# Kernel optimization log

Measured on AMD Instinct MI355X. Metric: run time of the kernel, lower is better.

## Reference

```python
import jax, jax.numpy as jnp
import numpy as np

H, B, S, D, T = 4, 16, 2048, 128, 5  # n_head, batch, seq_len, d_model, num event types
BAND_K = 64  # latest-k band width, as in get_latest_k_mask


def setup_inputs() -> dict:
    key = jax.random.key(0)
    ks = jax.random.split(key, 5)
    output = jax.random.normal(ks[0], (B, S, D), dtype=jnp.float32)
    # banded 'latest-k' mask: mask[i, i:i+k] = 1  (start=max(i,i-k+1)=i, end=min(S,i+k))
    i = jnp.arange(S)
    band = ((i[None, :] >= i[:, None]) & (i[None, :] < i[:, None] + BAND_K)).astype(jnp.float32)
    local_cor = band[None]  # [1, S, S]
    cor_matrix = jax.random.normal(ks[1], (T, D), dtype=jnp.float32)
    event_type = jax.random.randint(ks[2], (B, S), 1, T + 1)  # 1-based event ids in [1, T]
    # per-head linear3 params (xavier-ish); self.linear is unused in forward
    W3 = jax.random.normal(ks[3], (H, D, D), dtype=jnp.float32) / np.sqrt(D)
    b3 = jnp.zeros((H, D), dtype=jnp.float32)
    return dict(output=output, local_cor=local_cor, cor_matrix=cor_matrix,
                event_type=event_type, W3=W3, b3=b3)


def reference(output, local_cor, cor_matrix, event_type, W3, b3):
    # (corr^T @ cor_matrix[et-1]).mean(2) == einsum('bsd,bs->bd', corr, cor_matrix[et-1].mean(-1))
    g = cor_matrix.mean(-1)[event_type - 1]  # [B, S]
    x = output
    sum_seq = jnp.zeros_like(output)          # sum over heads of [B,S,D]
    sum_head = jnp.zeros((output.shape[0], output.shape[2]), output.dtype)  # [B,D]
    for h in range(H):
        z = jax.nn.elu(jnp.einsum('bsd,ed->bse', x, W3[h]) + b3[h])  # linear3 + ELU
        corr = jnp.matmul(local_cor, z)       # [1,S,S] @ [B,S,D] -> [B,S,D]
        head_out = jnp.einsum('bsd,bs->bd', corr, g)  # [B,D]
        sum_seq = sum_seq + corr
        sum_head = sum_head + head_out
        x = corr                               # next head consumes correlation_output
    return (sum_seq, sum_head)
```

## Files before the change

### kernel.cpp

```cpp
#include <hip/hip_runtime.h>
#include <math.h>

#define NHEAD 4
#define BATCH 16
#define SEQ   2048
#define DMODEL 128
#define NTYPES 5
#define BAND  64
#define MROWS (BATCH * SEQ)

typedef __attribute__((ext_vector_type(8))) short bf16x8;
typedef __attribute__((ext_vector_type(4))) float f32x4;
typedef __attribute__((ext_vector_type(4))) unsigned int u32x4;

static __device__ __forceinline__ unsigned short f2bf(float f) {
  unsigned int u = __float_as_uint(f);
  unsigned int r = (u + 0x7fffu + ((u >> 16) & 1u)) >> 16;
  return (unsigned short)r;
}
static __device__ __forceinline__ float bflo(unsigned int v) {
  return __uint_as_float(v << 16);
}
static __device__ __forceinline__ float bfhi(unsigned int v) {
  return __uint_as_float(v & 0xffff0000u);
}
static __device__ __forceinline__ unsigned int pkbf(float lo, float hi) {
  return ((unsigned int)f2bf(hi) << 16) | (unsigned int)f2bf(lo);
}
static __device__ __forceinline__ int xcd_swz(int blk, int nwg) {
  return (blk & 7) * (nwg >> 3) + (blk >> 3);
}

__global__ __launch_bounds__(512, 4) void gemm0_kernel(
    const float* __restrict__ X0,
    const float* __restrict__ W3h,
    const float* __restrict__ bvec,
    unsigned short* __restrict__ Zb,
    float* __restrict__ SH) {
  __shared__ __align__(16) char lds[64 * 272 + 128 * 272];
  char* Xl = lds;
  char* Wl = lds + 64 * 272;
  const int tid = threadIdx.x;
  const int swz = xcd_swz(blockIdx.x, gridDim.x);
  const int row0 = swz * 64;

  if (blockIdx.x < 16 && tid < DMODEL) SH[blockIdx.x * DMODEL + tid] = 0.f;

  #pragma unroll
  for (int it = 0; it < 2; ++it) {
    const int u = it * 512 + tid;
    const int r = u >> 4, g4 = u & 15;
    const float* xs = X0 + (long)(row0 + r) * DMODEL + g4 * 8;
    float4 f0 = *reinterpret_cast<const float4*>(xs);
    float4 f1 = *reinterpret_cast<const float4*>(xs + 4);
    unsigned short o[8];
    o[0] = f2bf(f0.x); o[1] = f2bf(f0.y); o[2] = f2bf(f0.z); o[3] = f2bf(f0.w);
    o[4] = f2bf(f1.x); o[5] = f2bf(f1.y); o[6] = f2bf(f1.z); o[7] = f2bf(f1.w);
    *reinterpret_cast<u32x4*>(Xl + r * 272 + g4 * 16) = *reinterpret_cast<u32x4*>(o);
  }
  #pragma unroll
  for (int it = 0; it < 4; ++it) {
    const int u = it * 512 + tid;
    const int e = u >> 4, g4 = u & 15;
    const float* wsrc = W3h + e * DMODEL + g4 * 8;
    float4 f0 = *reinterpret_cast<const float4*>(wsrc);
    float4 f1 = *reinterpret_cast<const float4*>(wsrc + 4);
    unsigned short o[8];
    o[0] = f2bf(f0.x); o[1] = f2bf(f0.y); o[2] = f2bf(f0.z); o[3] = f2bf(f0.w);
    o[4] = f2bf(f1.x); o[5] = f2bf(f1.y); o[6] = f2bf(f1.z); o[7] = f2bf(f1.w);
    *reinterpret_cast<u32x4*>(Wl + e * 272 + g4 * 16) = *reinterpret_cast<u32x4*>(o);
  }
  __syncthreads();

  const int wv = tid >> 6, l = tid & 63;
  const int mv = wv >> 1, nh = wv & 1;
  const int lr = l & 15, lk = l >> 4;
  f32x4 acc[4];
  #pragma unroll
  for (int n = 0; n < 4; ++n) acc[n] = (f32x4){0.f, 0.f, 0.f, 0.f};
  #pragma unroll
  for (int t = 0; t < 4; ++t) {
    const bf16x8 a = *reinterpret_cast<const bf16x8*>(
        Xl + (mv * 16 + lr) * 272 + (t * 4 + lk) * 16);
    #pragma unroll
    for (int n = 0; n < 4; ++n) {
      const bf16x8 bfrag = *reinterpret_cast<const bf16x8*>(
          Wl + (nh * 64 + n * 16 + lr) * 272 + (t * 4 + lk) * 16);
      acc[n] = __builtin_amdgcn_mfma_f32_16x16x32_bf16(a, bfrag, acc[n], 0, 0, 0);
    }
  }
  #pragma unroll
  for (int n = 0; n < 4; ++n) {
    const int col = nh * 64 + n * 16 + lr;
    const float bias = bvec[col];
    #pragma unroll
    for (int r = 0; r < 4; ++r) {
      const int row = row0 + mv * 16 + lk * 4 + r;
      float v = acc[n][r] + bias;
      const float e = expm1f(fminf(v, 0.f));
      v = v > 0.f ? v : e;
      Zb[(long)row * DMODEL + col] = f2bf(v);
    }
  }
}

template <int ACC>
__global__ __launch_bounds__(512, 4) void fused_band_gemm(
    const unsigned short* __restrict__ Zin,
    const unsigned short* __restrict__ CSin,
    unsigned short* __restrict__ Cout,
    const float* __restrict__ W3h,
    const float* __restrict__ bvec,
    unsigned short* __restrict__ Zout,
    float* __restrict__ SH,
    const int* __restrict__ et,
    const float* __restrict__ corm) {
  __shared__ __align__(16) char lds[56320];
  __shared__ float g_lds[64];
  __shared__ float rowmean[NTYPES];
  char* Xl = lds;
  char* Wl = lds + 17408;
  float2* s8 = reinterpret_cast<float2*>(lds + 17408);
  float* hred = reinterpret_cast<float*>(lds + 52224);

  const int tid = threadIdx.x;
  const int swz = xcd_swz(blockIdx.x, gridDim.x);
  const int r0 = swz * 64;
  const int b = r0 >> 11, s0 = r0 & 2047;
  const int p = tid & 63, q = tid >> 6;

  const unsigned int* zsrc =
      reinterpret_cast<const unsigned int*>(Zin) + (long)b * SEQ * 64 + p;
  unsigned int zlo[8], zhi[8];
  #pragma unroll
  for (int i = 0; i < 8; ++i) {
    const int sl = s0 + q * 8 + i;
    zlo[i] = zsrc[(long)sl * 64];
    const int sh_ = sl + BAND;
    zhi[i] = (sh_ < SEQ) ? zsrc[(long)sh_ * 64] : 0u;
  }
  unsigned int csr[8];
  if (ACC) {
    #pragma unroll
    for (int i = 0; i < 8; ++i)
      csr[i] = *reinterpret_cast<const unsigned int*>(
          CSin + ((long)r0 + q * 8 + i) * DMODEL + 2 * p);
  }
  u32x4 wfr[4];
  #pragma unroll
  for (int it = 0; it < 4; ++it) {
    const int u = it * 512 + tid;
    const int e = u >> 4, g4 = u & 15;
    const float* wsrc = W3h + e * DMODEL + g4 * 8;
    float4 f0 = *reinterpret_cast<const float4*>(wsrc);
    float4 f1 = *reinterpret_cast<const float4*>(wsrc + 4);
    unsigned short o[8];
    o[0] = f2bf(f0.x); o[1] = f2bf(f0.y); o[2] = f2bf(f0.z); o[3] = f2bf(f0.w);
    o[4] = f2bf(f1.x); o[5] = f2bf(f1.y); o[6] = f2bf(f1.z); o[7] = f2bf(f1.w);
    wfr[it] = *reinterpret_cast<u32x4*>(o);
  }
  int etv = 1;
  if (tid < 64) etv = et[(long)b * SEQ + s0 + tid];
  if (tid < 64) {
    #pragma unroll
    for (int t = 0; t < NTYPES; ++t) {
      float v = corm[t * DMODEL + tid] + corm[t * DMODEL + 64 + tid];
      #pragma unroll
      for (int o = 32; o > 0; o >>= 1) v += __shfl_xor(v, o, 64);
      if (tid == 0) rowmean[t] = v * (1.0f / DMODEL);
    }
  }

  {
    float a0 = 0.f, a1 = 0.f, b0 = 0.f, b1 = 0.f;
    #pragma unroll
    for (int i = 0; i < 8; ++i) {
      a0 += bflo(zlo[i]); a1 += bfhi(zlo[i]);
      b0 += bflo(zhi[i]); b1 += bfhi(zhi[i]);
    }
    s8[q * 64 + p] = make_float2(a0, a1);
    s8[(q + 8) * 64 + p] = make_float2(b0, b1);
  }
  __syncthreads();

  float w0 = 0.f, w1 = 0.f;
  #pragma unroll
  for (int j = 0; j < 8; ++j) {
    const float2 v = s8[(q + j) * 64 + p];
    w0 += v.x; w1 += v.y;
  }
  if (tid < 64) g_lds[tid] = rowmean[etv - 1];
  __syncthreads();

  #pragma unroll
  for (int it = 0; it < 4; ++it) {
    const int u = it * 512 + tid;
    const int e = u >> 4, g4 = u & 15;
    *reinterpret_cast<u32x4*>(Wl + e * 272 + g4 * 16) = wfr[it];
  }
  float hs0 = 0.f, hs1 = 0.f;
  #pragma unroll
  for (int i = 0; i < 8; ++i) {
    const int s = q * 8 + i;
    const float c0v = w0, c1v = w1;
    const float g = g_lds[s];
    hs0 += c0v * g; hs1 += c1v * g;
    unsigned int pk;
    if (ACC)
      pk = pkbf(c0v + bflo(csr[i]), c1v + bfhi(csr[i]));
    else
      pk = pkbf(c0v, c1v);
    *reinterpret_cast<unsigned int*>(Cout + ((long)r0 + s) * DMODEL + 2 * p) = pk;
    *reinterpret_cast<unsigned int*>(Xl + s * 272 + p * 4) =
        ACC ? pkbf(c0v, c1v) : pk;
    w0 += bflo(zhi[i]) - bflo(zlo[i]);
    w1 += bfhi(zhi[i]) - bfhi(zlo[i]);
  }
  *reinterpret_cast<float2*>(hred + (p * 8 + q) * 2) = make_float2(hs0, hs1);
  __syncthreads();

  if (q == 0) {
    float t0 = 0.f, t1 = 0.f;
    #pragma unroll
    for (int k = 0; k < 8; ++k) {
      const float2 v = *reinterpret_cast<const float2*>(hred + (p * 8 + k) * 2);
      t0 += v.x; t1 += v.y;
    }
    atomicAdd(SH + b * DMODEL + 2 * p, t0);
    atomicAdd(SH + b * DMODEL + 2 * p + 1, t1);
  }
  const int wv = tid >> 6, l = tid & 63;
  const int mv = wv >> 1, nh = wv & 1;
  const int lr = l & 15, lk = l >> 4;
  f32x4 acc[4];
  #pragma unroll
  for (int n = 0; n < 4; ++n) acc[n] = (f32x4){0.f, 0.f, 0.f, 0.f};
  #pragma unroll
  for (int t = 0; t < 4; ++t) {
    const bf16x8 a = *reinterpret_cast<const bf16x8*>(
        Xl + (mv * 16 + lr) * 272 + (t * 4 + lk) * 16);
    #pragma unroll
    for (int n = 0; n < 4; ++n) {
      const bf16x8 bfrag = *reinterpret_cast<const bf16x8*>(
          Wl + (nh * 64 + n * 16 + lr) * 272 + (t * 4 + lk) * 16);
      acc[n] = __builtin_amdgcn_mfma_f32_16x16x32_bf16(a, bfrag, acc[n], 0, 0, 0);
    }
  }
  #pragma unroll
  for (int n = 0; n < 4; ++n) {
    const int col = nh * 64 + n * 16 + lr;
    const float bias = bvec[col];
    #pragma unroll
    for (int r = 0; r < 4; ++r) {
      const int row = r0 + mv * 16 + lk * 4 + r;
      float v = acc[n][r] + bias;
      const float e = expm1f(fminf(v, 0.f));
      v = v > 0.f ? v : e;
      Zout[(long)row * DMODEL + col] = f2bf(v);
    }
  }
}

__global__ __launch_bounds__(512, 4) void band3_kernel(
    const unsigned short* __restrict__ Zin,
    const unsigned short* __restrict__ CSin,
    float* __restrict__ SS,
    float* __restrict__ SH,
    const int* __restrict__ et,
    const float* __restrict__ corm) {
  __shared__ float2 s8[16 * 64];
  __shared__ float hred[64 * 8 * 2];
  __shared__ float g_lds[64];
  __shared__ float rowmean[NTYPES];

  const int tid = threadIdx.x;
  const int swz = xcd_swz(blockIdx.x, gridDim.x);
  const int r0 = swz * 64;
  const int b = r0 >> 11, s0 = r0 & 2047;
  const int p = tid & 63, q = tid >> 6;

  const unsigned int* zsrc =
      reinterpret_cast<const unsigned int*>(Zin) + (long)b * SEQ * 64 + p;
  unsigned int zlo[8], zhi[8], csr[8];
  #pragma unroll
  for (int i = 0; i < 8; ++i) {
    const int sl = s0 + q * 8 + i;
    zlo[i] = zsrc[(long)sl * 64];
    const int sh_ = sl + BAND;
    zhi[i] = (sh_ < SEQ) ? zsrc[(long)sh_ * 64] : 0u;
    csr[i] = *reinterpret_cast<const unsigned int*>(
        CSin + ((long)r0 + q * 8 + i) * DMODEL + 2 * p);
  }
  int etv = 1;
  if (tid < 64) etv = et[(long)b * SEQ + s0 + tid];
  if (tid < 64) {
    #pragma unroll
    for (int t = 0; t < NTYPES; ++t) {
      float v = corm[t * DMODEL + tid] + corm[t * DMODEL + 64 + tid];
      #pragma unroll
      for (int o = 32; o > 0; o >>= 1) v += __shfl_xor(v, o, 64);
      if (tid == 0) rowmean[t] = v * (1.0f / DMODEL);
    }
  }
  {
    float a0 = 0.f, a1 = 0.f, b0 = 0.f, b1 = 0.f;
    #pragma unroll
    for (int i = 0; i < 8; ++i) {
      a0 += bflo(zlo[i]); a1 += bfhi(zlo[i]);
      b0 += bflo(zhi[i]); b1 += bfhi(zhi[i]);
    }
    s8[q * 64 + p] = make_float2(a0, a1);
    s8[(q + 8) * 64 + p] = make_float2(b0, b1);
  }
  __syncthreads();

  float w0 = 0.f, w1 = 0.f;
  #pragma unroll
  for (int j = 0; j < 8; ++j) {
    const float2 v = s8[(q + j) * 64 + p];
    w0 += v.x; w1 += v.y;
  }
  if (tid < 64) g_lds[tid] = rowmean[etv - 1];
  __syncthreads();

  float hs0 = 0.f, hs1 = 0.f;
  #pragma unroll
  for (int i = 0; i < 8; ++i) {
    const int s = q * 8 + i;
    const float c0v = w0, c1v = w1;
    const float g = g_lds[s];
    hs0 += c0v * g; hs1 += c1v * g;
    float2 o;
    o.x = c0v + bflo(csr[i]);
    o.y = c1v + bfhi(csr[i]);
    *reinterpret_cast<float2*>(SS + ((long)r0 + s) * DMODEL + 2 * p) = o;
    w0 += bflo(zhi[i]) - bflo(zlo[i]);
    w1 += bfhi(zhi[i]) - bfhi(zlo[i]);
  }
  *reinterpret_cast<float2*>(hred + (p * 8 + q) * 2) = make_float2(hs0, hs1);
  __syncthreads();
  if (q == 0) {
    float t0 = 0.f, t1 = 0.f;
    #pragma unroll
    for (int k = 0; k < 8; ++k) {
      const float2 v = *reinterpret_cast<const float2*>(hred + (p * 8 + k) * 2);
      t0 += v.x; t1 += v.y;
    }
    atomicAdd(SH + b * DMODEL + 2 * p, t0);
    atomicAdd(SH + b * DMODEL + 2 * p + 1, t1);
  }
}

extern "C" void kernel_launch(void* const* d_in, const int* in_sizes, int n_in,
                              void* d_out, int out_size, void* d_ws, size_t ws_size,
                              hipStream_t stream) {
  const float* x0   = (const float*)d_in[0];
  const float* corm = (const float*)d_in[2];
  const int*   et   = (const int*)d_in[3];
  const float* W3   = (const float*)d_in[4];
  const float* b3   = (const float*)d_in[5];

  float* out_ss = (float*)d_out;
  float* out_sh = out_ss + (size_t)MROWS * DMODEL;

  char* ws = (char*)d_ws;
  const size_t MB = 1024 * 1024;
  unsigned short* A = (unsigned short*)(ws + 0 * MB);
  unsigned short* B = (unsigned short*)(ws + 8 * MB);
  unsigned short* C = (unsigned short*)(ws + 16 * MB);
  unsigned short* D = (unsigned short*)(ws + 24 * MB);
  unsigned short* E = (unsigned short*)(ws + 32 * MB);

  const size_t WSTR = (size_t)DMODEL * DMODEL;

  gemm0_kernel<<<512, 512, 0, stream>>>(x0, W3, b3, A, out_sh);
  fused_band_gemm<0><<<512, 512, 0, stream>>>(
      A, nullptr, B, W3 + 1 * WSTR, b3 + 1 * DMODEL, E, out_sh, et, corm);
  fused_band_gemm<1><<<512, 512, 0, stream>>>(
      E, B, C, W3 + 2 * WSTR, b3 + 2 * DMODEL, A, out_sh, et, corm);
  fused_band_gemm<1><<<512, 512, 0, stream>>>(
      A, C, D, W3 + 3 * WSTR, b3 + 3 * DMODEL, E, out_sh, et, corm);
  band3_kernel<<<512, 512, 0, stream>>>(E, D, out_ss, out_sh, et, corm);
}
```

Baseline: 62.12 us.

## Pre-convert W3 to bf16 once and halve band-kernel tile to 32 rows

```diff
diff --git a/kernel.cpp b/kernel.cpp
--- a/kernel.cpp
+++ b/kernel.cpp
@@ -33,10 +33,11 @@
 
 __global__ __launch_bounds__(512, 4) void gemm0_kernel(
     const float* __restrict__ X0,
-    const float* __restrict__ W3h,
+    const float* __restrict__ W3,
     const float* __restrict__ bvec,
     unsigned short* __restrict__ Zb,
-    float* __restrict__ SH) {
+    float* __restrict__ SH,
+    unsigned short* __restrict__ wbf) {
   __shared__ __align__(16) char lds[64 * 272 + 128 * 272];
   char* Xl = lds;
   char* Wl = lds + 64 * 272;
@@ -45,6 +46,15 @@
   const int row0 = swz * 64;
 
   if (blockIdx.x < 16 && tid < DMODEL) SH[blockIdx.x * DMODEL + tid] = 0.f;
+  if (blockIdx.x < 12) {
+    const long u = (long)(blockIdx.x * 512 + tid) * 8 + DMODEL * DMODEL;
+    float4 a = *reinterpret_cast<const float4*>(W3 + u);
+    float4 c = *reinterpret_cast<const float4*>(W3 + u + 4);
+    unsigned short o[8];
+    o[0] = f2bf(a.x); o[1] = f2bf(a.y); o[2] = f2bf(a.z); o[3] = f2bf(a.w);
+    o[4] = f2bf(c.x); o[5] = f2bf(c.y); o[6] = f2bf(c.z); o[7] = f2bf(c.w);
+    *reinterpret_cast<u32x4*>(wbf + u) = *reinterpret_cast<u32x4*>(o);
+  }
 
   #pragma unroll
   for (int it = 0; it < 2; ++it) {
@@ -62,7 +72,7 @@
   for (int it = 0; it < 4; ++it) {
     const int u = it * 512 + tid;
     const int e = u >> 4, g4 = u & 15;
-    const float* wsrc = W3h + e * DMODEL + g4 * 8;
+    const float* wsrc = W3 + e * DMODEL + g4 * 8;
     float4 f0 = *reinterpret_cast<const float4*>(wsrc);
     float4 f1 = *reinterpret_cast<const float4*>(wsrc + 4);
     unsigned short o[8];
@@ -105,39 +115,38 @@
 }
 
 template <int ACC>
-__global__ __launch_bounds__(512, 4) void fused_band_gemm(
+__global__ __launch_bounds__(256, 4) void fused_band_gemm(
     const unsigned short* __restrict__ Zin,
     const unsigned short* __restrict__ CSin,
     unsigned short* __restrict__ Cout,
-    const float* __restrict__ W3h,
+    const unsigned short* __restrict__ Wb,
     const float* __restrict__ bvec,
     unsigned short* __restrict__ Zout,
     float* __restrict__ SH,
     const int* __restrict__ et,
     const float* __restrict__ corm) {
-  __shared__ __align__(16) char lds[56320];
-  __shared__ float g_lds[64];
+  __shared__ __align__(16) char Xl[32 * 272];
+  __shared__ float2 s8[12 * 64];
+  __shared__ float hred[64 * 4 * 2];
   __shared__ float rowmean[NTYPES];
-  char* Xl = lds;
-  char* Wl = lds + 17408;
-  float2* s8 = reinterpret_cast<float2*>(lds + 17408);
-  float* hred = reinterpret_cast<float*>(lds + 52224);
 
   const int tid = threadIdx.x;
   const int swz = xcd_swz(blockIdx.x, gridDim.x);
-  const int r0 = swz * 64;
+  const int r0 = swz * 32;
   const int b = r0 >> 11, s0 = r0 & 2047;
   const int p = tid & 63, q = tid >> 6;
 
   const unsigned int* zsrc =
       reinterpret_cast<const unsigned int*>(Zin) + (long)b * SEQ * 64 + p;
-  unsigned int zlo[8], zhi[8];
+  unsigned int za[8], zb[8], zc[8];
+  int etr[8];
   #pragma unroll
   for (int i = 0; i < 8; ++i) {
-    const int sl = s0 + q * 8 + i;
-    zlo[i] = zsrc[(long)sl * 64];
-    const int sh_ = sl + BAND;
-    zhi[i] = (sh_ < SEQ) ? zsrc[(long)sh_ * 64] : 0u;
+    const int s = s0 + q * 8 + i;
+    za[i] = zsrc[(long)s * 64];
+    zb[i] = (s + 32 < SEQ) ? zsrc[(long)(s + 32) * 64] : 0u;
+    zc[i] = (s + 64 < SEQ) ? zsrc[(long)(s + 64) * 64] : 0u;
+    etr[i] = et[(long)b * SEQ + s];
   }
   unsigned int csr[8];
   if (ACC) {
@@ -146,21 +155,6 @@
       csr[i] = *reinterpret_cast<const unsigned int*>(
           CSin + ((long)r0 + q * 8 + i) * DMODEL + 2 * p);
   }
-  u32x4 wfr[4];
-  #pragma unroll
-  for (int it = 0; it < 4; ++it) {
-    const int u = it * 512 + tid;
-    const int e = u >> 4, g4 = u & 15;
-    const float* wsrc = W3h + e * DMODEL + g4 * 8;
-    float4 f0 = *reinterpret_cast<const float4*>(wsrc);
-    float4 f1 = *reinterpret_cast<const float4*>(wsrc + 4);
-    unsigned short o[8];
-    o[0] = f2bf(f0.x); o[1] = f2bf(f0.y); o[2] = f2bf(f0.z); o[3] = f2bf(f0.w);
-    o[4] = f2bf(f1.x); o[5] = f2bf(f1.y); o[6] = f2bf(f1.z); o[7] = f2bf(f1.w);
-    wfr[it] = *reinterpret_cast<u32x4*>(o);
-  }
-  int etv = 1;
-  if (tid < 64) etv = et[(long)b * SEQ + s0 + tid];
   if (tid < 64) {
     #pragma unroll
     for (int t = 0; t < NTYPES; ++t) {
@@ -172,14 +166,16 @@
   }
 
   {
-    float a0 = 0.f, a1 = 0.f, b0 = 0.f, b1 = 0.f;
+    float a0 = 0.f, a1 = 0.f, b0 = 0.f, b1 = 0.f, c0 = 0.f, c1 = 0.f;
     #pragma unroll
     for (int i = 0; i < 8; ++i) {
-      a0 += bflo(zlo[i]); a1 += bfhi(zlo[i]);
-      b0 += bflo(zhi[i]); b1 += bfhi(zhi[i]);
+      a0 += bflo(za[i]); a1 += bfhi(za[i]);
+      b0 += bflo(zb[i]); b1 += bfhi(zb[i]);
+      c0 += bflo(zc[i]); c1 += bfhi(zc[i]);
     }
     s8[q * 64 + p] = make_float2(a0, a1);
-    s8[(q + 8) * 64 + p] = make_float2(b0, b1);
+    s8[(q + 4) * 64 + p] = make_float2(b0, b1);
+    s8[(q + 8) * 64 + p] = make_float2(c0, c1);
   }
   __syncthreads();
 
@@ -189,21 +185,12 @@
     const float2 v = s8[(q + j) * 64 + p];
     w0 += v.x; w1 += v.y;
   }
-  if (tid < 64) g_lds[tid] = rowmean[etv - 1];
-  __syncthreads();
-
-  #pragma unroll
-  for (int it = 0; it < 4; ++it) {
-    const int u = it * 512 + tid;
-    const int e = u >> 4, g4 = u & 15;
-    *reinterpret_cast<u32x4*>(Wl + e * 272 + g4 * 16) = wfr[it];
-  }
   float hs0 = 0.f, hs1 = 0.f;
   #pragma unroll
   for (int i = 0; i < 8; ++i) {
     const int s = q * 8 + i;
     const float c0v = w0, c1v = w1;
-    const float g = g_lds[s];
+    const float g = rowmean[etr[i] - 1];
     hs0 += c0v * g; hs1 += c1v * g;
     unsigned int pk;
     if (ACC)
@@ -213,47 +200,45 @@
     *reinterpret_cast<unsigned int*>(Cout + ((long)r0 + s) * DMODEL + 2 * p) = pk;
     *reinterpret_cast<unsigned int*>(Xl + s * 272 + p * 4) =
         ACC ? pkbf(c0v, c1v) : pk;
-    w0 += bflo(zhi[i]) - bflo(zlo[i]);
-    w1 += bfhi(zhi[i]) - bfhi(zlo[i]);
-  }
-  *reinterpret_cast<float2*>(hred + (p * 8 + q) * 2) = make_float2(hs0, hs1);
+    w0 += bflo(zc[i]) - bflo(za[i]);
+    w1 += bfhi(zc[i]) - bfhi(za[i]);
+  }
+  *reinterpret_cast<float2*>(hred + (p * 4 + q) * 2) = make_float2(hs0, hs1);
   __syncthreads();
 
   if (q == 0) {
     float t0 = 0.f, t1 = 0.f;
     #pragma unroll
-    for (int k = 0; k < 8; ++k) {
-      const float2 v = *reinterpret_cast<const float2*>(hred + (p * 8 + k) * 2);
+    for (int k = 0; k < 4; ++k) {
+      const float2 v = *reinterpret_cast<const float2*>(hred + (p * 4 + k) * 2);
       t0 += v.x; t1 += v.y;
     }
     atomicAdd(SH + b * DMODEL + 2 * p, t0);
     atomicAdd(SH + b * DMODEL + 2 * p + 1, t1);
   }
-  const int wv = tid >> 6, l = tid & 63;
-  const int mv = wv >> 1, nh = wv & 1;
-  const int lr = l & 15, lk = l >> 4;
-  f32x4 acc[4];
-  #pragma unroll
-  for (int n = 0; n < 4; ++n) acc[n] = (f32x4){0.f, 0.f, 0.f, 0.f};
-  #pragma unroll
-  for (int t = 0; t < 4; ++t) {
-    const bf16x8 a = *reinterpret_cast<const bf16x8*>(
-        Xl + (mv * 16 + lr) * 272 + (t * 4 + lk) * 16);
-    #pragma unroll
-    for (int n = 0; n < 4; ++n) {
+  const int mw = q >> 1, nw = q & 1;
+  const int lr = tid & 15, lk = (tid & 63) >> 4;
+  bf16x8 a[4];
+  #pragma unroll
+  for (int t = 0; t < 4; ++t)
+    a[t] = *reinterpret_cast<const bf16x8*>(
+        Xl + (mw * 16 + lr) * 272 + (t * 4 + lk) * 16);
+  #pragma unroll
+  for (int n = 0; n < 4; ++n) {
+    const int col0 = nw * 64 + n * 16;
+    f32x4 acc = (f32x4){0.f, 0.f, 0.f, 0.f};
+    #pragma unroll
+    for (int t = 0; t < 4; ++t) {
       const bf16x8 bfrag = *reinterpret_cast<const bf16x8*>(
-          Wl + (nh * 64 + n * 16 + lr) * 272 + (t * 4 + lk) * 16);
-      acc[n] = __builtin_amdgcn_mfma_f32_16x16x32_bf16(a, bfrag, acc[n], 0, 0, 0);
-    }
-  }
-  #pragma unroll
-  for (int n = 0; n < 4; ++n) {
-    const int col = nh * 64 + n * 16 + lr;
+          Wb + (long)(col0 + lr) * DMODEL + (t * 4 + lk) * 8);
+      acc = __builtin_amdgcn_mfma_f32_16x16x32_bf16(a[t], bfrag, acc, 0, 0, 0);
+    }
+    const int col = col0 + lr;
     const float bias = bvec[col];
     #pragma unroll
     for (int r = 0; r < 4; ++r) {
-      const int row = r0 + mv * 16 + lk * 4 + r;
-      float v = acc[n][r] + bias;
+      const int row = r0 + mw * 16 + lk * 4 + r;
+      float v = acc[r] + bias;
       const float e = expm1f(fminf(v, 0.f));
       v = v > 0.f ? v : e;
       Zout[(long)row * DMODEL + col] = f2bf(v);
@@ -261,38 +246,37 @@
   }
 }
 
-__global__ __launch_bounds__(512, 4) void band3_kernel(
+__global__ __launch_bounds__(256, 4) void band3_kernel(
     const unsigned short* __restrict__ Zin,
     const unsigned short* __restrict__ CSin,
     float* __restrict__ SS,
     float* __restrict__ SH,
     const int* __restrict__ et,
     const float* __restrict__ corm) {
-  __shared__ float2 s8[16 * 64];
-  __shared__ float hred[64 * 8 * 2];
-  __shared__ float g_lds[64];
+  __shared__ float2 s8[12 * 64];
+  __shared__ float hred[64 * 4 * 2];
   __shared__ float rowmean[NTYPES];
 
   const int tid = threadIdx.x;
   const int swz = xcd_swz(blockIdx.x, gridDim.x);
-  const int r0 = swz * 64;
+  const int r0 = swz * 32;
   const int b = r0 >> 11, s0 = r0 & 2047;
   const int p = tid & 63, q = tid >> 6;
 
   const unsigned int* zsrc =
       reinterpret_cast<const unsigned int*>(Zin) + (long)b * SEQ * 64 + p;
-  unsigned int zlo[8], zhi[8], csr[8];
+  unsigned int za[8], zb[8], zc[8], csr[8];
+  int etr[8];
   #pragma unroll
   for (int i = 0; i < 8; ++i) {
-    const int sl = s0 + q * 8 + i;
-    zlo[i] = zsrc[(long)sl * 64];
-    const int sh_ = sl + BAND;
-    zhi[i] = (sh_ < SEQ) ? zsrc[(long)sh_ * 64] : 0u;
+    const int s = s0 + q * 8 + i;
+    za[i] = zsrc[(long)s * 64];
+    zb[i] = (s + 32 < SEQ) ? zsrc[(long)(s + 32) * 64] : 0u;
+    zc[i] = (s + 64 < SEQ) ? zsrc[(long)(s + 64) * 64] : 0u;
+    etr[i] = et[(long)b * SEQ + s];
     csr[i] = *reinterpret_cast<const unsigned int*>(
         CSin + ((long)r0 + q * 8 + i) * DMODEL + 2 * p);
   }
-  int etv = 1;
-  if (tid < 64) etv = et[(long)b * SEQ + s0 + tid];
   if (tid < 64) {
     #pragma unroll
     for (int t = 0; t < NTYPES; ++t) {
@@ -303,14 +287,16 @@
     }
   }
   {
-    float a0 = 0.f, a1 = 0.f, b0 = 0.f, b1 = 0.f;
+    float a0 = 0.f, a1 = 0.f, b0 = 0.f, b1 = 0.f, c0 = 0.f, c1 = 0.f;
     #pragma unroll
     for (int i = 0; i < 8; ++i) {
-      a0 += bflo(zlo[i]); a1 += bfhi(zlo[i]);
-      b0 += bflo(zhi[i]); b1 += bfhi(zhi[i]);
+      a0 += bflo(za[i]); a1 += bfhi(za[i]);
+      b0 += bflo(zb[i]); b1 += bfhi(zb[i]);
+      c0 += bflo(zc[i]); c1 += bfhi(zc[i]);
     }
     s8[q * 64 + p] = make_float2(a0, a1);
-    s8[(q + 8) * 64 + p] = make_float2(b0, b1);
+    s8[(q + 4) * 64 + p] = make_float2(b0, b1);
+    s8[(q + 8) * 64 + p] = make_float2(c0, c1);
   }
   __syncthreads();
 
@@ -320,30 +306,27 @@
     const float2 v = s8[(q + j) * 64 + p];
     w0 += v.x; w1 += v.y;
   }
-  if (tid < 64) g_lds[tid] = rowmean[etv - 1];
-  __syncthreads();
-
   float hs0 = 0.f, hs1 = 0.f;
   #pragma unroll
   for (int i = 0; i < 8; ++i) {
     const int s = q * 8 + i;
     const float c0v = w0, c1v = w1;
-    const float g = g_lds[s];
+    const float g = rowmean[etr[i] - 1];
     hs0 += c0v * g; hs1 += c1v * g;
     float2 o;
     o.x = c0v + bflo(csr[i]);
     o.y = c1v + bfhi(csr[i]);
     *reinterpret_cast<float2*>(SS + ((long)r0 + s) * DMODEL + 2 * p) = o;
-    w0 += bflo(zhi[i]) - bflo(zlo[i]);
-    w1 += bfhi(zhi[i]) - bfhi(zlo[i]);
-  }
-  *reinterpret_cast<float2*>(hred + (p * 8 + q) * 2) = make_float2(hs0, hs1);
+    w0 += bflo(zc[i]) - bflo(za[i]);
+    w1 += bfhi(zc[i]) - bfhi(za[i]);
+  }
+  *reinterpret_cast<float2*>(hred + (p * 4 + q) * 2) = make_float2(hs0, hs1);
   __syncthreads();
   if (q == 0) {
     float t0 = 0.f, t1 = 0.f;
     #pragma unroll
-    for (int k = 0; k < 8; ++k) {
-      const float2 v = *reinterpret_cast<const float2*>(hred + (p * 8 + k) * 2);
+    for (int k = 0; k < 4; ++k) {
+      const float2 v = *reinterpret_cast<const float2*>(hred + (p * 4 + k) * 2);
       t0 += v.x; t1 += v.y;
     }
     atomicAdd(SH + b * DMODEL + 2 * p, t0);
@@ -370,15 +353,16 @@
   unsigned short* C = (unsigned short*)(ws + 16 * MB);
   unsigned short* D = (unsigned short*)(ws + 24 * MB);
   unsigned short* E = (unsigned short*)(ws + 32 * MB);
+  unsigned short* wbf = (unsigned short*)(ws + 40 * MB);
 
   const size_t WSTR = (size_t)DMODEL * DMODEL;
 
-  gemm0_kernel<<<512, 512, 0, stream>>>(x0, W3, b3, A, out_sh);
-  fused_band_gemm<0><<<512, 512, 0, stream>>>(
-      A, nullptr, B, W3 + 1 * WSTR, b3 + 1 * DMODEL, E, out_sh, et, corm);
-  fused_band_gemm<1><<<512, 512, 0, stream>>>(
-      E, B, C, W3 + 2 * WSTR, b3 + 2 * DMODEL, A, out_sh, et, corm);
-  fused_band_gemm<1><<<512, 512, 0, stream>>>(
-      A, C, D, W3 + 3 * WSTR, b3 + 3 * DMODEL, E, out_sh, et, corm);
-  band3_kernel<<<512, 512, 0, stream>>>(E, D, out_ss, out_sh, et, corm);
-}
+  gemm0_kernel<<<512, 512, 0, stream>>>(x0, W3, b3, A, out_sh, wbf);
+  fused_band_gemm<0><<<1024, 256, 0, stream>>>(
+      A, nullptr, B, wbf + 1 * WSTR, b3 + 1 * DMODEL, E, out_sh, et, corm);
+  fused_band_gemm<1><<<1024, 256, 0, stream>>>(
+      E, B, C, wbf + 2 * WSTR, b3 + 2 * DMODEL, A, out_sh, et, corm);
+  fused_band_gemm<1><<<1024, 256, 0, stream>>>(
+      A, C, D, wbf + 3 * WSTR, b3 + 3 * DMODEL, E, out_sh, et, corm);
+  band3_kernel<<<1024, 256, 0, stream>>>(E, D, out_ss, out_sh, et, corm);
+}
```

After: 76.88 us. 1.24x slower.

## Pre-convert head weights to bf16 once, load per-row event types directly

Applied to the files above, without the earlier changes.

```diff
diff --git a/kernel.cpp b/kernel.cpp
--- a/kernel.cpp
+++ b/kernel.cpp
@@ -27,16 +27,21 @@
 static __device__ __forceinline__ unsigned int pkbf(float lo, float hi) {
   return ((unsigned int)f2bf(hi) << 16) | (unsigned int)f2bf(lo);
 }
+static __device__ __forceinline__ float elu(float v) {
+  const float ev = __expf(fminf(v, 0.f)) - 1.f;
+  return v > 0.f ? v : ev;
+}
 static __device__ __forceinline__ int xcd_swz(int blk, int nwg) {
   return (blk & 7) * (nwg >> 3) + (blk >> 3);
 }
 
 __global__ __launch_bounds__(512, 4) void gemm0_kernel(
     const float* __restrict__ X0,
-    const float* __restrict__ W3h,
+    const float* __restrict__ W3,
     const float* __restrict__ bvec,
     unsigned short* __restrict__ Zb,
-    float* __restrict__ SH) {
+    float* __restrict__ SH,
+    unsigned short* __restrict__ wbf) {
   __shared__ __align__(16) char lds[64 * 272 + 128 * 272];
   char* Xl = lds;
   char* Wl = lds + 64 * 272;
@@ -45,6 +50,15 @@
   const int row0 = swz * 64;
 
   if (blockIdx.x < 16 && tid < DMODEL) SH[blockIdx.x * DMODEL + tid] = 0.f;
+  if (blockIdx.x < 12) {
+    const long u = (long)(blockIdx.x * 512 + tid) * 8 + DMODEL * DMODEL;
+    float4 a = *reinterpret_cast<const float4*>(W3 + u);
+    float4 c = *reinterpret_cast<const float4*>(W3 + u + 4);
+    unsigned short o[8];
+    o[0] = f2bf(a.x); o[1] = f2bf(a.y); o[2] = f2bf(a.z); o[3] = f2bf(a.w);
+    o[4] = f2bf(c.x); o[5] = f2bf(c.y); o[6] = f2bf(c.z); o[7] = f2bf(c.w);
+    *reinterpret_cast<u32x4*>(wbf + u) = *reinterpret_cast<u32x4*>(o);
+  }
 
   #pragma unroll
   for (int it = 0; it < 2; ++it) {
@@ -62,7 +76,7 @@
   for (int it = 0; it < 4; ++it) {
     const int u = it * 512 + tid;
     const int e = u >> 4, g4 = u & 15;
-    const float* wsrc = W3h + e * DMODEL + g4 * 8;
+    const float* wsrc = W3 + e * DMODEL + g4 * 8;
     float4 f0 = *reinterpret_cast<const float4*>(wsrc);
     float4 f1 = *reinterpret_cast<const float4*>(wsrc + 4);
     unsigned short o[8];
@@ -96,10 +110,7 @@
     #pragma unroll
     for (int r = 0; r < 4; ++r) {
       const int row = row0 + mv * 16 + lk * 4 + r;
-      float v = acc[n][r] + bias;
-      const float e = expm1f(fminf(v, 0.f));
-      v = v > 0.f ? v : e;
-      Zb[(long)row * DMODEL + col] = f2bf(v);
+      Zb[(long)row * DMODEL + col] = f2bf(elu(acc[n][r] + bias));
     }
   }
 }
@@ -109,19 +120,18 @@
     const unsigned short* __restrict__ Zin,
     const unsigned short* __restrict__ CSin,
     unsigned short* __restrict__ Cout,
-    const float* __restrict__ W3h,
+    const unsigned short* __restrict__ Wb,
     const float* __restrict__ bvec,
     unsigned short* __restrict__ Zout,
     float* __restrict__ SH,
     const int* __restrict__ et,
     const float* __restrict__ corm) {
-  __shared__ __align__(16) char lds[56320];
-  __shared__ float g_lds[64];
-  __shared__ float rowmean[NTYPES];
+  __shared__ __align__(16) char lds[64512];
   char* Xl = lds;
   char* Wl = lds + 17408;
-  float2* s8 = reinterpret_cast<float2*>(lds + 17408);
-  float* hred = reinterpret_cast<float*>(lds + 52224);
+  float2* s8 = reinterpret_cast<float2*>(lds + 52224);
+  float* hred = reinterpret_cast<float*>(lds + 60416);
+  float* rowmean = reinterpret_cast<float*>(Xl + 256);
 
   const int tid = threadIdx.x;
   const int swz = xcd_swz(blockIdx.x, gridDim.x);
@@ -132,12 +142,14 @@
   const unsigned int* zsrc =
       reinterpret_cast<const unsigned int*>(Zin) + (long)b * SEQ * 64 + p;
   unsigned int zlo[8], zhi[8];
+  int etr[8];
   #pragma unroll
   for (int i = 0; i < 8; ++i) {
     const int sl = s0 + q * 8 + i;
     zlo[i] = zsrc[(long)sl * 64];
     const int sh_ = sl + BAND;
     zhi[i] = (sh_ < SEQ) ? zsrc[(long)sh_ * 64] : 0u;
+    etr[i] = et[(long)b * SEQ + sl];
   }
   unsigned int csr[8];
   if (ACC) {
@@ -146,31 +158,22 @@
       csr[i] = *reinterpret_cast<const unsigned int*>(
           CSin + ((long)r0 + q * 8 + i) * DMODEL + 2 * p);
   }
-  u32x4 wfr[4];
   #pragma unroll
   for (int it = 0; it < 4; ++it) {
     const int u = it * 512 + tid;
     const int e = u >> 4, g4 = u & 15;
-    const float* wsrc = W3h + e * DMODEL + g4 * 8;
-    float4 f0 = *reinterpret_cast<const float4*>(wsrc);
-    float4 f1 = *reinterpret_cast<const float4*>(wsrc + 4);
-    unsigned short o[8];
-    o[0] = f2bf(f0.x); o[1] = f2bf(f0.y); o[2] = f2bf(f0.z); o[3] = f2bf(f0.w);
-    o[4] = f2bf(f1.x); o[5] = f2bf(f1.y); o[6] = f2bf(f1.z); o[7] = f2bf(f1.w);
-    wfr[it] = *reinterpret_cast<u32x4*>(o);
-  }
-  int etv = 1;
-  if (tid < 64) etv = et[(long)b * SEQ + s0 + tid];
+    u32x4 v = *reinterpret_cast<const u32x4*>(Wb + e * DMODEL + g4 * 8);
+    *reinterpret_cast<u32x4*>(Wl + e * 272 + g4 * 16) = v;
+  }
   if (tid < 64) {
     #pragma unroll
     for (int t = 0; t < NTYPES; ++t) {
       float v = corm[t * DMODEL + tid] + corm[t * DMODEL + 64 + tid];
       #pragma unroll
       for (int o = 32; o > 0; o >>= 1) v += __shfl_xor(v, o, 64);
-      if (tid == 0) rowmean[t] = v * (1.0f / DMODEL);
-    }
-  }
-
+      if (tid == 0) rowmean[t * 68] = v * (1.0f / DMODEL);
+    }
+  }
   {
     float a0 = 0.f, a1 = 0.f, b0 = 0.f, b1 = 0.f;
     #pragma unroll
@@ -189,21 +192,12 @@
     const float2 v = s8[(q + j) * 64 + p];
     w0 += v.x; w1 += v.y;
   }
-  if (tid < 64) g_lds[tid] = rowmean[etv - 1];
-  __syncthreads();
-
-  #pragma unroll
-  for (int it = 0; it < 4; ++it) {
-    const int u = it * 512 + tid;
-    const int e = u >> 4, g4 = u & 15;
-    *reinterpret_cast<u32x4*>(Wl + e * 272 + g4 * 16) = wfr[it];
-  }
   float hs0 = 0.f, hs1 = 0.f;
   #pragma unroll
   for (int i = 0; i < 8; ++i) {
     const int s = q * 8 + i;
     const float c0v = w0, c1v = w1;
-    const float g = g_lds[s];
+    const float g = rowmean[(etr[i] - 1) * 68];
     hs0 += c0v * g; hs1 += c1v * g;
     unsigned int pk;
     if (ACC)
@@ -253,10 +247,7 @@
     #pragma unroll
     for (int r = 0; r < 4; ++r) {
       const int row = r0 + mv * 16 + lk * 4 + r;
-      float v = acc[n][r] + bias;
-      const float e = expm1f(fminf(v, 0.f));
-      v = v > 0.f ? v : e;
-      Zout[(long)row * DMODEL + col] = f2bf(v);
+      Zout[(long)row * DMODEL + col] = f2bf(elu(acc[n][r] + bias));
     }
   }
 }
@@ -270,7 +261,6 @@
     const float* __restrict__ corm) {
   __shared__ float2 s8[16 * 64];
   __shared__ float hred[64 * 8 * 2];
-  __shared__ float g_lds[64];
   __shared__ float rowmean[NTYPES];
 
   const int tid = threadIdx.x;
@@ -282,17 +272,17 @@
   const unsigned int* zsrc =
       reinterpret_cast<const unsigned int*>(Zin) + (long)b * SEQ * 64 + p;
   unsigned int zlo[8], zhi[8], csr[8];
+  int etr[8];
   #pragma unroll
   for (int i = 0; i < 8; ++i) {
     const int sl = s0 + q * 8 + i;
     zlo[i] = zsrc[(long)sl * 64];
     const int sh_ = sl + BAND;
     zhi[i] = (sh_ < SEQ) ? zsrc[(long)sh_ * 64] : 0u;
+    etr[i] = et[(long)b * SEQ + sl];
     csr[i] = *reinterpret_cast<const unsigned int*>(
         CSin + ((long)r0 + q * 8 + i) * DMODEL + 2 * p);
   }
-  int etv = 1;
-  if (tid < 64) etv = et[(long)b * SEQ + s0 + tid];
   if (tid < 64) {
     #pragma unroll
     for (int t = 0; t < NTYPES; ++t) {
@@ -320,15 +310,12 @@
     const float2 v = s8[(q + j) * 64 + p];
     w0 += v.x; w1 += v.y;
   }
-  if (tid < 64) g_lds[tid] = rowmean[etv - 1];
-  __syncthreads();
-
   float hs0 = 0.f, hs1 = 0.f;
   #pragma unroll
   for (int i = 0; i < 8; ++i) {
     const int s = q * 8 + i;
     const float c0v = w0, c1v = w1;
-    const float g = g_lds[s];
+    const float g = rowmean[etr[i] - 1];
     hs0 += c0v * g; hs1 += c1v * g;
     float2 o;
     o.x = c0v + bflo(csr[i]);
@@ -370,15 +357,16 @@
   unsigned short* C = (unsigned short*)(ws + 16 * MB);
   unsigned short* D = (unsigned short*)(ws + 24 * MB);
   unsigned short* E = (unsigned short*)(ws + 32 * MB);
+  unsigned short* wbf = (unsigned short*)(ws + 40 * MB);
 
   const size_t WSTR = (size_t)DMODEL * DMODEL;
 
-  gemm0_kernel<<<512, 512, 0, stream>>>(x0, W3, b3, A, out_sh);
+  gemm0_kernel<<<512, 512, 0, stream>>>(x0, W3, b3, A, out_sh, wbf);
   fused_band_gemm<0><<<512, 512, 0, stream>>>(
-      A, nullptr, B, W3 + 1 * WSTR, b3 + 1 * DMODEL, E, out_sh, et, corm);
+      A, nullptr, B, wbf + 1 * WSTR, b3 + 1 * DMODEL, E, out_sh, et, corm);
   fused_band_gemm<1><<<512, 512, 0, stream>>>(
-      E, B, C, W3 + 2 * WSTR, b3 + 2 * DMODEL, A, out_sh, et, corm);
+      E, B, C, wbf + 2 * WSTR, b3 + 2 * DMODEL, A, out_sh, et, corm);
   fused_band_gemm<1><<<512, 512, 0, stream>>>(
-      A, C, D, W3 + 3 * WSTR, b3 + 3 * DMODEL, E, out_sh, et, corm);
+      A, C, D, wbf + 3 * WSTR, b3 + 3 * DMODEL, E, out_sh, et, corm);
   band3_kernel<<<512, 512, 0, stream>>>(E, D, out_ss, out_sh, et, corm);
 }
```

After: 55.22 us. 1.12x faster.
